# Optimization experiments

Hardware: AMD Instinct MI355X
Metric: run time of the kernel (lower is better)

The kernel has to match this reference:

```python
import jax, jax.numpy as jnp
import numpy as np

HEADS = 64
DIM_HEAD = 64
SCALE = DIM_HEAD ** -0.5
EPS = 1e-6


def setup_inputs() -> dict:
    key = jax.random.key(0)
    ks = jax.random.split(key, 6)
    b, s, dim = 2, 4096, 1024
    inner = HEADS * DIM_HEAD  # 4096
    std = 0.02
    return {
        "x": jax.random.normal(ks[0], (b, s, dim), dtype=jnp.float32),
        "Wq": jax.random.normal(ks[1], (dim, inner), dtype=jnp.float32) * std,
        "Wk": jax.random.normal(ks[2], (dim, inner), dtype=jnp.float32) * std,
        "Wv": jax.random.normal(ks[3], (dim, inner), dtype=jnp.float32) * std,
        "Wo": jax.random.normal(ks[4], (inner, dim), dtype=jnp.float32) * std,
        "bo": jnp.zeros((dim,), dtype=jnp.float32),
    }


def reference(x, Wq, Wk, Wv, Wo, bo):
    b, s, dim = x.shape
    h, dh = HEADS, DIM_HEAD
    # projections -> [b, s, h, dh]
    q = (x @ Wq).reshape(b, s, h, dh)
    k = (x @ Wk).reshape(b, s, h, dh)
    v = (x @ Wv).reshape(b, s, h, dh)
    # kernel feature map (relu) + scale on q
    q = jax.nn.relu(q) * SCALE
    k = jax.nn.relu(k)
    # NOTE: faithful to the source, these einsums contract over the HEAD axis
    # per token (i, j index heads; d indexes dim_head).
    kv = jnp.einsum('bsid,bsjd->bsdj', k, v)          # [b, s, dh, h]
    out = jnp.einsum('bsid,bsdj->bsij', q, kv)        # [b, s, h, h]
    q_norm = jnp.einsum('bsid,bsd->bsi', q, k.sum(axis=2))  # [b, s, h]
    out = out / (q_norm[..., None] + EPS)
    out = out.reshape(b, s, h * h)                    # h*h == h*dh since h == dh
    return out @ Wo + bo
```

## Files before the change

kernel.cpp:

```cpp
#include <hip/hip_runtime.h>
#include <hip/hip_bf16.h>
#include <cstdint>

#define M_TOK 8192
#define DIM   1024
#define INNER 4096
#define HEADS 64
#define DH    64
#define QSCALE 0.125f
#define EPS    1e-6f

typedef __hip_bfloat16 bf16;
typedef __bf16 bf16x8_t __attribute__((ext_vector_type(8)));
typedef float f32x4_t __attribute__((ext_vector_type(4)));

__device__ __forceinline__ float bfbits2f(unsigned short u) {
  return __uint_as_float(((unsigned)u) << 16);
}
__device__ __forceinline__ unsigned short f2bfbits(float f) {
  __hip_bfloat16 h = __float2bfloat16(f);
  unsigned short u;
  __builtin_memcpy(&u, &h, 2);
  return u;
}

__device__ __forceinline__ void load_lds16(const void* g, void* l) {
  __builtin_amdgcn_global_load_lds(
      (__attribute__((address_space(1))) void*)g,
      (__attribute__((address_space(3))) void*)l, 16, 0, 0);
}

__device__ __forceinline__ void asm_barrier() {
  asm volatile("s_barrier" ::: "memory");
}

#define LGKM_SB(N) do { \
    asm volatile("s_waitcnt lgkmcnt(" #N ")" ::: "memory"); \
    __builtin_amdgcn_sched_barrier(0); } while (0)

__device__ __forceinline__ void swizzle_xy(int& bx, int& by) {
  const int gx = gridDim.x, gy = gridDim.y;
  const int id  = blockIdx.x + gx * blockIdx.y;
  const int per = gy >> 3;
  const int xcd = id & 7;
  const int s   = id >> 3;
  by = xcd * per + (s % per);
  bx = s / per;
}

__global__ __launch_bounds__(256) void prep_kernel(
    const float* __restrict__ x, unsigned short* __restrict__ xb,
    const float* __restrict__ Wk, const float* __restrict__ Wv,
    unsigned short* __restrict__ WtKV)
{
  const int bid = blockIdx.x;
  if (bid < 8192) {
    const int i = bid * 256 + threadIdx.x;
    const float4 v = reinterpret_cast<const float4*>(x)[i];
    ushort4 o;
    o.x = f2bfbits(v.x); o.y = f2bfbits(v.y);
    o.z = f2bfbits(v.z); o.w = f2bfbits(v.w);
    reinterpret_cast<ushort4*>(xb)[i] = o;
    return;
  }
  __shared__ float tile[32][33];
  const int t    = bid - 8192;
  const int z    = t >> 12;
  const int tt   = t & 4095;
  const float* W = z ? Wv : Wk;
  unsigned short* dst = WtKV + (size_t)z * DIM * INNER;
  const int bx = (tt & 127) * 32;
  const int by = (tt >> 7) * 32;
  const int tx = threadIdx.x & 31;
  const int ty = threadIdx.x >> 5;
#pragma unroll
  for (int k = 0; k < 4; ++k)
    tile[ty + k * 8][tx] = W[(size_t)(by + ty + k * 8) * INNER + bx + tx];
  __syncthreads();
#pragma unroll
  for (int k = 0; k < 4; ++k) {
    const int c  = bx + ty + k * 8;
    const int rp = z ? c : (((c & 63) << 6) | (c >> 6));
    dst[(size_t)rp * DIM + by + tx] = f2bfbits(tile[tx][ty + k * 8]);
  }
}

__global__ __launch_bounds__(256) void tcast_kernel(
    const float* __restrict__ W, unsigned short* __restrict__ Wt, int R, int C)
{
  __shared__ float tile[32][33];
  const int bx = blockIdx.x * 32;
  const int by = blockIdx.y * 32;
  const int tx = threadIdx.x & 31;
  const int ty = threadIdx.x >> 5;
#pragma unroll
  for (int k = 0; k < 4; ++k)
    tile[ty + k * 8][tx] = W[(size_t)(by + ty + k * 8) * C + bx + tx];
  __syncthreads();
#pragma unroll
  for (int k = 0; k < 4; ++k)
    Wt[(size_t)(bx + ty + k * 8) * R + by + tx] = f2bfbits(tile[tx][ty + k * 8]);
}

__device__ __forceinline__ void stage_half(
    const unsigned short* __restrict__ G, unsigned short* L,
    int rowbase, int k0, int K, int h, int tid)
{
#pragma unroll
  for (int j = 0; j < 2; ++j) {
    const int q  = h * 1024 + j * 512 + tid;
    const int r  = q >> 3;
    const int cg = (tid & 7) ^ (r & 7);
    load_lds16(&G[(size_t)(rowbase + r) * K + k0 + cg * 8], &L[q * 8]);
  }
}

__device__ __forceinline__ void read_af4(
    const unsigned short* __restrict__ Ac, bf16x8_t (&af)[8][2],
    int m0, int wm, int l15, int quad)
{
#pragma unroll
  for (int mt = 0; mt < 4; ++mt) {
    const int r = wm + (m0 + mt) * 16 + l15;
#pragma unroll
    for (int kt = 0; kt < 2; ++kt) {
      const int s = (kt * 4 + quad) ^ (r & 7);
      af[m0 + mt][kt] = *reinterpret_cast<const bf16x8_t*>(&Ac[r * 64 + s * 8]);
    }
  }
}

__device__ __forceinline__ void read_bf2(
    const unsigned short* __restrict__ Bc, bf16x8_t (&bfr)[4][2],
    int n0, int wn, int l15, int quad)
{
#pragma unroll
  for (int nt = 0; nt < 2; ++nt) {
    const int r = wn + (n0 + nt) * 16 + l15;
#pragma unroll
    for (int kt = 0; kt < 2; ++kt) {
      const int s = (kt * 4 + quad) ^ (r & 7);
      bfr[n0 + nt][kt] = *reinterpret_cast<const bf16x8_t*>(&Bc[r * 64 + s * 8]);
    }
  }
}

__device__ __forceinline__ void mfma_quad(
    f32x4_t (&acc)[8][4], const bf16x8_t (&af)[8][2],
    const bf16x8_t (&bfr)[4][2], int m0, int n0)
{
  __builtin_amdgcn_s_setprio(1);
#pragma unroll
  for (int mt = m0; mt < m0 + 4; ++mt)
#pragma unroll
    for (int nt = n0; nt < n0 + 2; ++nt) {
      acc[mt][nt] = __builtin_amdgcn_mfma_f32_16x16x32_bf16(
          af[mt][0], bfr[nt][0], acc[mt][nt], 0, 0, 0);
      acc[mt][nt] = __builtin_amdgcn_mfma_f32_16x16x32_bf16(
          af[mt][1], bfr[nt][1], acc[mt][nt], 0, 0, 0);
    }
  __builtin_amdgcn_s_setprio(0);
}

template <int MODE, int DUAL>
__global__ __launch_bounds__(512, 2) void gemm256(
    const unsigned short* __restrict__ A,
    const unsigned short* __restrict__ Bt,
    unsigned short* __restrict__ C0,
    unsigned short* __restrict__ C1,
    float* __restrict__ ks,
    int N, int K)
{
  __shared__ __align__(16) unsigned short As[2][256 * 64];
  __shared__ __align__(16) unsigned short Bs[2][256 * 64];

  int bxi, byi;
  swizzle_xy(bxi, byi);
  const int tid  = threadIdx.x;
  const int bm   = byi * 256;
  const int bn   = bxi * 256;
  const int lane = tid & 63;
  const int w    = tid >> 6;
  const int wm   = (w >> 2) * 128;
  const int wn   = (w & 3) * 64;
  const int quad = lane >> 4;
  const int l15  = lane & 15;

  f32x4_t acc[8][4];
#pragma unroll
  for (int mt = 0; mt < 8; ++mt)
#pragma unroll
    for (int nt = 0; nt < 4; ++nt) acc[mt][nt] = (f32x4_t){0.f, 0.f, 0.f, 0.f};

  const int NT = K >> 6;

  bf16x8_t af[8][2], bfr[4][2];

  stage_half(A,  As[0], bm, 0,  K, 0, tid);
  stage_half(A,  As[0], bm, 0,  K, 1, tid);
  stage_half(Bt, Bs[0], bn, 0,  K, 0, tid);
  stage_half(Bt, Bs[0], bn, 0,  K, 1, tid);
  stage_half(A,  As[1], bm, 64, K, 0, tid);
  stage_half(A,  As[1], bm, 64, K, 1, tid);
  asm volatile("s_waitcnt vmcnt(4)" ::: "memory");
  asm_barrier();
  __builtin_amdgcn_sched_barrier(0);
  read_af4(As[0], af, 0, wm, l15, quad);
  read_bf2(Bs[0], bfr, 0, wn, l15, quad);

  for (int T = 0; T < NT; ++T) {
    const int c = T & 1;
    const unsigned short* Ac = As[c];
    const unsigned short* Bc = Bs[c];
    unsigned short* Bnx = Bs[c ^ 1];
    unsigned short* Anx = As[c];
    const int kB = (T + 1) * 64;
    const int kA = (T + 2) * 64;
    const bool pB = (T + 1 < NT);
    const bool pA = (T + 2 < NT);

    read_af4(Ac, af, 4, wm, l15, quad);
    LGKM_SB(8);
    mfma_quad(acc, af, bfr, 0, 0);

    read_bf2(Bc, bfr, 2, wn, l15, quad);
    if (pB) stage_half(Bt, Bnx, bn, kB, K, 0, tid);
    LGKM_SB(4);
    mfma_quad(acc, af, bfr, 4, 0);

    if (pB) stage_half(Bt, Bnx, bn, kB, K, 1, tid);
    if (pA) stage_half(A, Anx, bm, kA, K, 0, tid);
    LGKM_SB(0);
    mfma_quad(acc, af, bfr, 0, 2);

    if (pA) stage_half(A, Anx, bm, kA, K, 1, tid);
    mfma_quad(acc, af, bfr, 4, 2);
    if (T < NT - 2) {
      asm volatile("s_waitcnt vmcnt(4)" ::: "memory");
    } else {
      asm volatile("s_waitcnt vmcnt(0)" ::: "memory");
    }
    asm_barrier();
    __builtin_amdgcn_sched_barrier(0);
    if (T + 1 < NT) {
      read_af4(As[c ^ 1], af, 0, wm, l15, quad);
      read_bf2(Bs[c ^ 1], bfr, 0, wn, l15, quad);
    }
  }

  if (DUAL) {
    if (bn < 4096) {
      const int dh = (bn + wn) >> 6;
#pragma unroll
      for (int mt = 0; mt < 8; ++mt)
#pragma unroll
        for (int i = 0; i < 4; ++i) {
          float s = 0.f;
#pragma unroll
          for (int nt = 0; nt < 4; ++nt) s += fmaxf(acc[mt][nt][i], 0.f);
          s += __shfl_xor(s, 1, 16);
          s += __shfl_xor(s, 2, 16);
          s += __shfl_xor(s, 4, 16);
          s += __shfl_xor(s, 8, 16);
          if (l15 == 0) {
            const size_t rowg = (size_t)(bm + wm + mt * 16 + quad * 4 + i);
            ks[rowg * 64 + dh] = s;
          }
        }
    } else {
      const int bnc = bn & 4095;
#pragma unroll
      for (int mt = 0; mt < 8; ++mt)
#pragma unroll
        for (int i = 0; i < 4; ++i) {
          const size_t rowg = (size_t)(bm + wm + mt * 16 + quad * 4 + i);
#pragma unroll
          for (int nt = 0; nt < 4; ++nt)
            C1[rowg * 4096 + bnc + wn + nt * 16 + l15] = f2bfbits(acc[mt][nt][i]);
        }
    }
  } else {
#pragma unroll
    for (int mt = 0; mt < 8; ++mt)
#pragma unroll
      for (int i = 0; i < 4; ++i) {
        const size_t rowg = (size_t)(bm + wm + mt * 16 + quad * 4 + i);
#pragma unroll
        for (int nt = 0; nt < 4; ++nt) {
          float v = acc[mt][nt][i];
          if (MODE >= 1) v = fmaxf(v, 0.f);
          if (MODE == 2) v *= QSCALE;
          C0[rowg * (size_t)N + bn + wn + nt * 16 + l15] = f2bfbits(v);
        }
      }
  }
}

__global__ __launch_bounds__(256) void gemm_out128(
    const unsigned short* __restrict__ A,
    const unsigned short* __restrict__ Bt,
    const float* __restrict__ bias,
    float* __restrict__ out, int N, int K)
{
  __shared__ __align__(16) unsigned short As[128 * 64];
  __shared__ __align__(16) unsigned short Bs[128 * 64];

  int bxi, byi;
  swizzle_xy(bxi, byi);
  const int tid  = threadIdx.x;
  const int bm   = byi * 128;
  const int bn   = bxi * 128;
  const int lane = tid & 63;
  const int w    = tid >> 6;
  const int wm   = (w & 1) * 64;
  const int wn   = (w >> 1) * 64;
  const int quad = lane >> 4;
  const int l15  = lane & 15;

  f32x4_t acc[4][4];
#pragma unroll
  for (int mt = 0; mt < 4; ++mt)
#pragma unroll
    for (int nt = 0; nt < 4; ++nt) acc[mt][nt] = (f32x4_t){0.f, 0.f, 0.f, 0.f};

  int qa[4], ra[4], ca[4];
#pragma unroll
  for (int j = 0; j < 4; ++j) {
    qa[j] = tid + 256 * j;
    ra[j] = qa[j] >> 3;
    ca[j] = (qa[j] & 7) ^ (ra[j] & 7);
  }

  for (int k0 = 0; k0 < K; k0 += 64) {
    __syncthreads();
#pragma unroll
    for (int j = 0; j < 4; ++j) {
      load_lds16(&A [(size_t)(bm + ra[j]) * K + k0 + ca[j] * 8], &As[qa[j] * 8]);
      load_lds16(&Bt[(size_t)(bn + ra[j]) * K + k0 + ca[j] * 8], &Bs[qa[j] * 8]);
    }
    __syncthreads();

    bf16x8_t af[4][2], bfr[4][2];
#pragma unroll
    for (int mt = 0; mt < 4; ++mt) {
      const int r = wm + mt * 16 + l15;
#pragma unroll
      for (int kt = 0; kt < 2; ++kt) {
        const int slot = (kt * 4 + quad) ^ (r & 7);
        af[mt][kt] = *reinterpret_cast<const bf16x8_t*>(&As[r * 64 + slot * 8]);
      }
    }
#pragma unroll
    for (int nt = 0; nt < 4; ++nt) {
      const int r = wn + nt * 16 + l15;
#pragma unroll
      for (int kt = 0; kt < 2; ++kt) {
        const int slot = (kt * 4 + quad) ^ (r & 7);
        bfr[nt][kt] = *reinterpret_cast<const bf16x8_t*>(&Bs[r * 64 + slot * 8]);
      }
    }
#pragma unroll
    for (int mt = 0; mt < 4; ++mt)
#pragma unroll
      for (int nt = 0; nt < 4; ++nt) {
        acc[mt][nt] = __builtin_amdgcn_mfma_f32_16x16x32_bf16(
            af[mt][0], bfr[nt][0], acc[mt][nt], 0, 0, 0);
        acc[mt][nt] = __builtin_amdgcn_mfma_f32_16x16x32_bf16(
            af[mt][1], bfr[nt][1], acc[mt][nt], 0, 0, 0);
      }
  }

#pragma unroll
  for (int mt = 0; mt < 4; ++mt)
#pragma unroll
    for (int i = 0; i < 4; ++i) {
      const size_t rowg = (size_t)(bm + wm + mt * 16 + quad * 4 + i);
#pragma unroll
      for (int nt = 0; nt < 4; ++nt) {
        const int colg = bn + wn + nt * 16 + l15;
        out[rowg * N + colg] = acc[mt][nt][i] + bias[colg];
      }
    }
}

__global__ __launch_bounds__(256) void attn_mfma(
    const unsigned short* __restrict__ Qb, const unsigned short* __restrict__ Vb,
    const float* __restrict__ ksum, unsigned short* __restrict__ Ab)
{
  const int t    = blockIdx.x * 4 + (threadIdx.x >> 6);
  const int lane = threadIdx.x & 63;
  const int l15  = lane & 15;
  const int quad = lane >> 4;
  const size_t base = (size_t)t * INNER;

  union VU { bf16x8_t v; unsigned short u[8]; };

  float ksv[2][8];
#pragma unroll
  for (int kt = 0; kt < 2; ++kt) {
    const float4* p = reinterpret_cast<const float4*>(ksum + t * 64 + kt * 32 + quad * 8);
    const float4 a = p[0], b = p[1];
    ksv[kt][0] = a.x; ksv[kt][1] = a.y; ksv[kt][2] = a.z; ksv[kt][3] = a.w;
    ksv[kt][4] = b.x; ksv[kt][5] = b.y; ksv[kt][6] = b.z; ksv[kt][7] = b.w;
  }

  bf16x8_t vs[4][2];
#pragma unroll
  for (int nt = 0; nt < 4; ++nt)
#pragma unroll
    for (int kt = 0; kt < 2; ++kt) {
      VU vr, vo;
      vr.v = *reinterpret_cast<const bf16x8_t*>(
          Vb + base + (size_t)(nt * 16 + l15) * 64 + kt * 32 + quad * 8);
#pragma unroll
      for (int j = 0; j < 8; ++j)
        vo.u[j] = f2bfbits(bfbits2f(vr.u[j]) * ksv[kt][j]);
      vs[nt][kt] = vo.v;
    }

  bf16x8_t qf[4][2];
  float qn[4] = {0.f, 0.f, 0.f, 0.f};
#pragma unroll
  for (int mt = 0; mt < 4; ++mt)
#pragma unroll
    for (int kt = 0; kt < 2; ++kt) {
      VU qr;
      qr.v = *reinterpret_cast<const bf16x8_t*>(
          Qb + base + (size_t)(mt * 16 + l15) * 64 + kt * 32 + quad * 8);
      qf[mt][kt] = qr.v;
#pragma unroll
      for (int j = 0; j < 8; ++j)
        qn[mt] += bfbits2f(qr.u[j]) * ksv[kt][j];
    }
#pragma unroll
  for (int mt = 0; mt < 4; ++mt) {
    qn[mt] += __shfl_xor(qn[mt], 16, 64);
    qn[mt] += __shfl_xor(qn[mt], 32, 64);
  }

  f32x4_t acc[4][4];
#pragma unroll
  for (int mt = 0; mt < 4; ++mt)
#pragma unroll
    for (int nt = 0; nt < 4; ++nt) acc[mt][nt] = (f32x4_t){0.f, 0.f, 0.f, 0.f};

#pragma unroll
  for (int mt = 0; mt < 4; ++mt)
#pragma unroll
    for (int nt = 0; nt < 4; ++nt) {
      acc[mt][nt] = __builtin_amdgcn_mfma_f32_16x16x32_bf16(
          qf[mt][0], vs[nt][0], acc[mt][nt], 0, 0, 0);
      acc[mt][nt] = __builtin_amdgcn_mfma_f32_16x16x32_bf16(
          qf[mt][1], vs[nt][1], acc[mt][nt], 0, 0, 0);
    }

#pragma unroll
  for (int mt = 0; mt < 4; ++mt)
#pragma unroll
    for (int i = 0; i < 4; ++i) {
      const float inv = 1.f / (__shfl(qn[mt], quad * 4 + i, 64) + EPS);
      const size_t roff = base + (size_t)(mt * 16 + quad * 4 + i) * 64;
#pragma unroll
      for (int nt = 0; nt < 4; ++nt)
        Ab[roff + nt * 16 + l15] = f2bfbits(acc[mt][nt][i] * inv);
    }
}

extern "C" void kernel_launch(void* const* d_in, const int* in_sizes, int n_in,
                              void* d_out, int out_size, void* d_ws, size_t ws_size,
                              hipStream_t stream)
{
  const float* x  = (const float*)d_in[0];
  const float* Wq = (const float*)d_in[1];
  const float* Wk = (const float*)d_in[2];
  const float* Wv = (const float*)d_in[3];
  const float* Wo = (const float*)d_in[4];
  const float* bo = (const float*)d_in[5];
  float* out = (float*)d_out;

  uint8_t* ws = (uint8_t*)d_ws;
  const size_t HALF = (size_t)M_TOK * INNER * sizeof(bf16);
  unsigned short* KQA = (unsigned short*)ws;
  unsigned short* Vb  = (unsigned short*)(ws + HALF);
  float* ks           = (float*)(ws + 2 * HALF);

  unsigned short* Xb   = (unsigned short*)d_out;
  unsigned short* WtKV = (unsigned short*)((uint8_t*)d_out + (16u << 20));
  unsigned short* WqT  = WtKV;
  unsigned short* Wot  = Vb;

  const dim3 blk(256);
  const dim3 blk512(512);

  prep_kernel<<<dim3(16384), blk, 0, stream>>>(x, Xb, Wk, Wv, WtKV);

  gemm256<0, 1><<<dim3(2 * INNER / 256, M_TOK / 256), blk512, 0, stream>>>(
      Xb, WtKV, nullptr, Vb, ks, 2 * INNER, DIM);

  tcast_kernel<<<dim3(INNER / 32, DIM / 32), blk, 0, stream>>>(
      Wq, WqT, DIM, INNER);

  gemm256<2, 0><<<dim3(INNER / 256, M_TOK / 256), blk512, 0, stream>>>(
      Xb, WqT, KQA, nullptr, nullptr, INNER, DIM);

  attn_mfma<<<dim3(M_TOK / 4), blk, 0, stream>>>(KQA, Vb, ks, KQA);

  tcast_kernel<<<dim3(DIM / 32, INNER / 32), blk, 0, stream>>>(
      Wo, Wot, INNER, DIM);

  gemm_out128<<<dim3(DIM / 128, M_TOK / 128), blk, 0, stream>>>(
      KQA, Wot, bo, out, DIM, INNER);
}
```

Measured before the change: 436.5 us.

## Replace output GEMM with 256x128 double-buffered pipelined kernel

Rewrites the final output projection GEMM to use 256x128 tiles with 512 threads, double-buffered LDS, and split prefetch of the next K-slices interleaved with MFMA halves. It reuses the staging and fragment-read helpers already used by the projection GEMMs. The aim is to hide global-to-LDS latency and raise data reuse per block compared with the old single-buffered 128x128 kernel. The cost is more LDS per block (96 KB) and more register pressure, and the grid halves to 256 blocks, which may reduce occupancy.

```diff
diff --git a/kernel.cpp b/kernel.cpp
--- a/kernel.cpp
+++ b/kernel.cpp
@@ -111,6 +111,19 @@
     const int q  = h * 1024 + j * 512 + tid;
     const int r  = q >> 3;
     const int cg = (tid & 7) ^ (r & 7);
+    load_lds16(&G[(size_t)(rowbase + r) * K + k0 + cg * 8], &L[q * 8]);
+  }
+}
+
+__device__ __forceinline__ void stage_b128(
+    const unsigned short* __restrict__ G, unsigned short* L,
+    int rowbase, int k0, int K, int tid)
+{
+#pragma unroll
+  for (int j = 0; j < 2; ++j) {
+    const int q  = j * 512 + tid;
+    const int r  = q >> 3;
+    const int cg = (q & 7) ^ (r & 7);
     load_lds16(&G[(size_t)(rowbase + r) * K + k0 + cg * 8], &L[q * 8]);
   }
 }
@@ -296,87 +309,126 @@
   }
 }
 
-__global__ __launch_bounds__(256) void gemm_out128(
+__global__ __launch_bounds__(512, 2) void gemm_out256(
     const unsigned short* __restrict__ A,
     const unsigned short* __restrict__ Bt,
     const float* __restrict__ bias,
     float* __restrict__ out, int N, int K)
 {
-  __shared__ __align__(16) unsigned short As[128 * 64];
-  __shared__ __align__(16) unsigned short Bs[128 * 64];
+  __shared__ __align__(16) unsigned short As[2][256 * 64];
+  __shared__ __align__(16) unsigned short Bs[2][128 * 64];
 
   int bxi, byi;
   swizzle_xy(bxi, byi);
   const int tid  = threadIdx.x;
-  const int bm   = byi * 128;
+  const int bm   = byi * 256;
   const int bn   = bxi * 128;
   const int lane = tid & 63;
   const int w    = tid >> 6;
-  const int wm   = (w & 1) * 64;
-  const int wn   = (w >> 1) * 64;
+  const int wm   = (w >> 2) * 128;
+  const int wn   = (w & 3) * 32;
   const int quad = lane >> 4;
   const int l15  = lane & 15;
 
-  f32x4_t acc[4][4];
-#pragma unroll
-  for (int mt = 0; mt < 4; ++mt)
-#pragma unroll
-    for (int nt = 0; nt < 4; ++nt) acc[mt][nt] = (f32x4_t){0.f, 0.f, 0.f, 0.f};
-
-  int qa[4], ra[4], ca[4];
-#pragma unroll
-  for (int j = 0; j < 4; ++j) {
-    qa[j] = tid + 256 * j;
-    ra[j] = qa[j] >> 3;
-    ca[j] = (qa[j] & 7) ^ (ra[j] & 7);
-  }
-
-  for (int k0 = 0; k0 < K; k0 += 64) {
-    __syncthreads();
-#pragma unroll
-    for (int j = 0; j < 4; ++j) {
-      load_lds16(&A [(size_t)(bm + ra[j]) * K + k0 + ca[j] * 8], &As[qa[j] * 8]);
-      load_lds16(&Bt[(size_t)(bn + ra[j]) * K + k0 + ca[j] * 8], &Bs[qa[j] * 8]);
-    }
-    __syncthreads();
-
-    bf16x8_t af[4][2], bfr[4][2];
-#pragma unroll
-    for (int mt = 0; mt < 4; ++mt) {
-      const int r = wm + mt * 16 + l15;
-#pragma unroll
-      for (int kt = 0; kt < 2; ++kt) {
-        const int slot = (kt * 4 + quad) ^ (r & 7);
-        af[mt][kt] = *reinterpret_cast<const bf16x8_t*>(&As[r * 64 + slot * 8]);
-      }
-    }
-#pragma unroll
-    for (int nt = 0; nt < 4; ++nt) {
-      const int r = wn + nt * 16 + l15;
-#pragma unroll
-      for (int kt = 0; kt < 2; ++kt) {
-        const int slot = (kt * 4 + quad) ^ (r & 7);
-        bfr[nt][kt] = *reinterpret_cast<const bf16x8_t*>(&Bs[r * 64 + slot * 8]);
-      }
-    }
+  f32x4_t acc[8][2];
+#pragma unroll
+  for (int mt = 0; mt < 8; ++mt)
+#pragma unroll
+    for (int nt = 0; nt < 2; ++nt) acc[mt][nt] = (f32x4_t){0.f, 0.f, 0.f, 0.f};
+
+  const int NT = K >> 6;
+
+  bf16x8_t af[8][2];
+  bf16x8_t bfr[2][2];
+
+  stage_half(A,  As[0], bm, 0,  K, 0, tid);
+  stage_half(A,  As[0], bm, 0,  K, 1, tid);
+  stage_b128(Bt, Bs[0], bn, 0,  K, tid);
+  stage_half(A,  As[1], bm, 64, K, 0, tid);
+  stage_half(A,  As[1], bm, 64, K, 1, tid);
+  asm volatile("s_waitcnt vmcnt(4)" ::: "memory");
+  asm_barrier();
+  __builtin_amdgcn_sched_barrier(0);
+  read_af4(As[0], af, 0, wm, l15, quad);
+#pragma unroll
+  for (int nt = 0; nt < 2; ++nt) {
+    const int r = wn + nt * 16 + l15;
+#pragma unroll
+    for (int kt = 0; kt < 2; ++kt) {
+      const int s = (kt * 4 + quad) ^ (r & 7);
+      bfr[nt][kt] = *reinterpret_cast<const bf16x8_t*>(&Bs[0][r * 64 + s * 8]);
+    }
+  }
+
+  for (int T = 0; T < NT; ++T) {
+    const int c = T & 1;
+    const unsigned short* Ac = As[c];
+    unsigned short* Bnx = Bs[c ^ 1];
+    unsigned short* Anx = As[c];
+    const int kB = (T + 1) * 64;
+    const int kA = (T + 2) * 64;
+    const bool pB = (T + 1 < NT);
+    const bool pA = (T + 2 < NT);
+
+    read_af4(Ac, af, 4, wm, l15, quad);
+    LGKM_SB(8);
+    __builtin_amdgcn_s_setprio(1);
 #pragma unroll
     for (int mt = 0; mt < 4; ++mt)
 #pragma unroll
-      for (int nt = 0; nt < 4; ++nt) {
+      for (int nt = 0; nt < 2; ++nt) {
         acc[mt][nt] = __builtin_amdgcn_mfma_f32_16x16x32_bf16(
             af[mt][0], bfr[nt][0], acc[mt][nt], 0, 0, 0);
         acc[mt][nt] = __builtin_amdgcn_mfma_f32_16x16x32_bf16(
             af[mt][1], bfr[nt][1], acc[mt][nt], 0, 0, 0);
       }
-  }
-
-#pragma unroll
-  for (int mt = 0; mt < 4; ++mt)
+    __builtin_amdgcn_s_setprio(0);
+
+    if (pB) stage_b128(Bt, Bnx, bn, kB, K, tid);
+    if (pA) stage_half(A, Anx, bm, kA, K, 0, tid);
+    LGKM_SB(0);
+    __builtin_amdgcn_s_setprio(1);
+#pragma unroll
+    for (int mt = 4; mt < 8; ++mt)
+#pragma unroll
+      for (int nt = 0; nt < 2; ++nt) {
+        acc[mt][nt] = __builtin_amdgcn_mfma_f32_16x16x32_bf16(
+            af[mt][0], bfr[nt][0], acc[mt][nt], 0, 0, 0);
+        acc[mt][nt] = __builtin_amdgcn_mfma_f32_16x16x32_bf16(
+            af[mt][1], bfr[nt][1], acc[mt][nt], 0, 0, 0);
+      }
+    __builtin_amdgcn_s_setprio(0);
+
+    if (pA) stage_half(A, Anx, bm, kA, K, 1, tid);
+    if (T < NT - 2) {
+      asm volatile("s_waitcnt vmcnt(4)" ::: "memory");
+    } else {
+      asm volatile("s_waitcnt vmcnt(0)" ::: "memory");
+    }
+    asm_barrier();
+    __builtin_amdgcn_sched_barrier(0);
+    if (T + 1 < NT) {
+      read_af4(As[c ^ 1], af, 0, wm, l15, quad);
+      const unsigned short* Bn = Bs[c ^ 1];
+#pragma unroll
+      for (int nt = 0; nt < 2; ++nt) {
+        const int r = wn + nt * 16 + l15;
+#pragma unroll
+        for (int kt = 0; kt < 2; ++kt) {
+          const int s = (kt * 4 + quad) ^ (r & 7);
+          bfr[nt][kt] = *reinterpret_cast<const bf16x8_t*>(&Bn[r * 64 + s * 8]);
+        }
+      }
+    }
+  }
+
+#pragma unroll
+  for (int mt = 0; mt < 8; ++mt)
 #pragma unroll
     for (int i = 0; i < 4; ++i) {
       const size_t rowg = (size_t)(bm + wm + mt * 16 + quad * 4 + i);
 #pragma unroll
-      for (int nt = 0; nt < 4; ++nt) {
+      for (int nt = 0; nt < 2; ++nt) {
         const int colg = bn + wn + nt * 16 + l15;
         out[rowg * N + colg] = acc[mt][nt][i] + bias[colg];
       }
@@ -508,6 +560,6 @@
   tcast_kernel<<<dim3(DIM / 32, INNER / 32), blk, 0, stream>>>(
       Wo, Wot, INNER, DIM);
 
-  gemm_out128<<<dim3(DIM / 128, M_TOK / 128), blk, 0, stream>>>(
+  gemm_out256<<<dim3(DIM / 128, M_TOK / 256), blk512, 0, stream>>>(
       KQA, Wot, bo, out, DIM, INNER);
 }
```

After: 440.2 us. Within noise of the previous version (+0.9%).
